# Kernel optimization log

Hardware: AMD Instinct MI355X
Metric: run time of the kernel (lower is better)

The kernel has to match this reference:

```python
import jax, jax.numpy as jnp
from jax import lax
import numpy as np

B, H, W = 8, 256, 256
NH = 128          # num_hiddens
NRH = 32          # num_residual_hiddens
K = 1024          # num_embeddings
D = 128           # embedding_dim
CC = 0.25         # commitment_cost


def setup_inputs() -> dict:
    key = jax.random.key(0)
    ks = jax.random.split(key, 18)

    def w(k, shape):
        fan_in = int(np.prod(shape[1:]))
        return (jax.random.normal(k, shape, jnp.float32) / np.sqrt(fan_in)).astype(jnp.float32)

    inp = {
        "x": jax.random.normal(ks[0], (B, 3, H, W), jnp.float32),
        # encoder
        "enc_c1": w(ks[1], (NH // 2, 3, 4, 4)),        # conv4x4 s2
        "enc_c2": w(ks[2], (NH, NH // 2, 4, 4)),       # conv4x4 s2
        "enc_c3": w(ks[3], (NH, NH, 3, 3)),            # conv3x3
        "enc_r1a": w(ks[4], (NRH, NH, 3, 3)),
        "enc_r1b": w(ks[5], (NH, NRH, 1, 1)),
        "enc_r2a": w(ks[6], (NRH, NH, 3, 3)),
        "enc_r2b": w(ks[7], (NH, NRH, 1, 1)),
        "pre_vq_w": w(ks[8], (D, NH, 1, 1)),
        # codebook: uniform(-1/K, 1/K) as in original init
        "codebook": jax.random.uniform(ks[9], (K, D), jnp.float32, -1.0 / K, 1.0 / K),
        # decoder
        "dec_c1": w(ks[10], (NH, D, 3, 3)),
        "dec_r1a": w(ks[11], (NRH, NH, 3, 3)),
        "dec_r1b": w(ks[12], (NH, NRH, 1, 1)),
        "dec_r2a": w(ks[13], (NRH, NH, 3, 3)),
        "dec_r2b": w(ks[14], (NH, NRH, 1, 1)),
        # ConvTranspose2d weight, torch layout [Cin, Cout, 4, 4]
        "dec_dc": w(ks[15], (NH, NH // 2, 4, 4)),
        "dec_c3": w(ks[16], (3, NH // 2, 3, 3)),
    }
    return inp


def _conv(x, w, s, p):
    return lax.conv_general_dilated(x, w, (s, s), ((p, p), (p, p)),
                                    dimension_numbers=("NCHW", "OIHW", "NCHW"))


def _deconv4x4_s2_p1(x, w_t):
    # torch ConvTranspose2d(k=4, s=2, p=1): flip kernel, swap in/out, lhs-dilate
    w = jnp.transpose(w_t[:, :, ::-1, ::-1], (1, 0, 2, 3))  # [Cout, Cin, 4, 4]
    return lax.conv_general_dilated(x, w, (1, 1), ((2, 2), (2, 2)),
                                    lhs_dilation=(2, 2),
                                    dimension_numbers=("NCHW", "OIHW", "NCHW"))


def _res_stack(x, r1a, r1b, r2a, r2b):
    for a, b in ((r1a, r1b), (r2a, r2b)):
        h = _conv(jax.nn.relu(x), a, 1, 1)
        h = _conv(jax.nn.relu(h), b, 1, 0)
        x = x + h
    return jax.nn.relu(x)


def _resize1d_align(x, axis, out_size):
    n = x.shape[axis]
    pos = jnp.arange(out_size, dtype=jnp.float32) * ((n - 1) / (out_size - 1))
    lo = jnp.floor(pos).astype(jnp.int32)
    hi = jnp.minimum(lo + 1, n - 1)
    wt = (pos - lo.astype(jnp.float32)).astype(x.dtype)
    shape = [1] * x.ndim
    shape[axis] = out_size
    wt = wt.reshape(shape)
    return jnp.take(x, lo, axis=axis) * (1 - wt) + jnp.take(x, hi, axis=axis) * wt


def _upsample2x_bilinear_align(x):  # align_corners=True, separable
    x = _resize1d_align(x, 2, 2 * x.shape[2])
    return _resize1d_align(x, 3, 2 * x.shape[3])


def reference(x, enc_c1, enc_c2, enc_c3, enc_r1a, enc_r1b, enc_r2a, enc_r2b,
              pre_vq_w, codebook, dec_c1, dec_r1a, dec_r1b, dec_r2a, dec_r2b,
              dec_dc, dec_c3):
    # ---- encoder ----
    h = jax.nn.relu(_conv(x, enc_c1, 2, 1))
    h = jax.nn.relu(_conv(h, enc_c2, 2, 1))
    h = _conv(h, enc_c3, 1, 1)            # note: no relu here (matches source)
    h = _res_stack(h, enc_r1a, enc_r1b, enc_r2a, enc_r2b)
    z = _conv(h, pre_vq_w, 1, 0)          # [B, D, H/4, W/4]

    # ---- VQ (eval mode: no EMA update, q_latent_loss = 0) ----
    zp = jnp.transpose(z, (0, 2, 3, 1))               # [B, h, w, D]
    flat = zp.reshape(-1, D)                          # [N, D]
    dist = (jnp.sum(flat * flat, axis=1, keepdims=True)
            + jnp.sum(codebook * codebook, axis=1)
            - 2.0 * flat @ codebook.T)                # [N, K]
    idx = jnp.argmin(dist, axis=1)                    # [N]
    q = codebook[idx].reshape(zp.shape)               # gather lookup
    e_latent_loss = jnp.mean((lax.stop_gradient(q) - zp) ** 2)
    loss = CC * e_latent_loss
    q_st = zp + lax.stop_gradient(q - zp)             # straight-through
    counts = jnp.zeros((K,), jnp.float32).at[idx].add(1.0)
    avg_probs = counts / flat.shape[0]
    perplexity = jnp.exp(-jnp.sum(avg_probs * jnp.log(avg_probs + 1e-10)))
    quantized = jnp.transpose(q_st, (0, 3, 1, 2))     # [B, D, h, w]

    # ---- decoder ----
    d = _conv(quantized, dec_c1, 1, 1)
    d = _res_stack(d, dec_r1a, dec_r1b, dec_r2a, dec_r2b)
    d = jax.nn.relu(_deconv4x4_s2_p1(d, dec_dc))
    d = _upsample2x_bilinear_align(d)
    d = _conv(d, dec_c3, 1, 1)
    recon = 2.0 * jax.nn.sigmoid(d) - 1.0             # [B, 3, H, W]
    return loss, recon, perplexity
```

## Files before the change

### kernel.cpp

```cpp
#include <hip/hip_runtime.h>
#include <hip/hip_bf16.h>
#include <math.h>

#define CC_COST 0.25

typedef __attribute__((ext_vector_type(8))) short short8v;
typedef __attribute__((ext_vector_type(4))) float f32x4;
typedef __attribute__((ext_vector_type(16))) float f32x16;

__device__ __forceinline__ unsigned short f2bf(float f) {
    unsigned u = __float_as_uint(f);
    unsigned r = (u + 0x7FFFu + ((u >> 16) & 1u)) >> 16;
    return (unsigned short)r;
}
__device__ __forceinline__ float bf2f(unsigned short h) {
    return __uint_as_float(((unsigned)h) << 16);
}


struct WtJobs {
    const float* src[15];
    float* dst[15];
    int cout[15], cin[15], kk[15], kind[15];
    int blk0[16];
};

__global__ void wt_batch_k(WtJobs J)
{
    int blk = blockIdx.x;
    int j = 0;
    while (j < 14 && blk >= J.blk0[j + 1]) ++j;
    int i = (blk - J.blk0[j]) * 256 + threadIdx.x;
    int total = J.cout[j] * J.cin[j] * J.kk[j];
    if (i >= total) return;
    const float* src = J.src[j];
    float* dst = J.dst[j];
    int kind = J.kind[j];
    if (kind == 0) {
        int Cout = J.cout[j], Cin = J.cin[j], KK = J.kk[j];
        int oc = i % Cout; int t2 = i / Cout; int t = t2 % KK; int c = t2 / KK;
        dst[i] = src[(oc * Cin + c) * KK + t];
    } else {
        int o = i % 3; int t = (i / 3) % 9; int c = i / 27;
        dst[i] = src[(o * 64 + c) * 9 + t];
    }
}

__global__ void wt_split_k(const float* __restrict__ w,
                           unsigned short* __restrict__ whi,
                           unsigned short* __restrict__ wlo)
{
    int i = blockIdx.x * 256 + threadIdx.x;
    if (i >= 147456) return;
    int ci = i & 15;
    int oc = (i >> 4) & 127;
    int rest = i >> 11;
    int cb = rest & 7;
    int tap = rest >> 3;
    float v = w[(oc * 128 + cb * 16 + ci) * 9 + tap];
    unsigned short h = f2bf(v);
    whi[i] = h;
    wlo[i] = f2bf(v - bf2f(h));
}

__global__ void wt_split4_k(const float* __restrict__ w,
                            unsigned short* __restrict__ whi,
                            unsigned short* __restrict__ wlo)
{
    int i = blockIdx.x * 256 + threadIdx.x;
    if (i >= 131072) return;
    int t = i & 15;
    int oc = (i >> 4) & 127;
    int rest = i >> 11;
    int cb = rest & 3;
    int tap = rest >> 2;
    float v = w[(oc * 64 + cb * 16 + t) * 16 + tap];
    unsigned short h = f2bf(v);
    whi[i] = h;
    wlo[i] = f2bf(v - bf2f(h));
}

__global__ void wt_split_dc_k(const float* __restrict__ w,
                              unsigned short* __restrict__ whi,
                              unsigned short* __restrict__ wlo)
{
    int i = blockIdx.x * 256 + threadIdx.x;
    if (i >= 131072) return;
    int ci = i & 15;
    int oc = (i >> 4) & 63;
    int cb = (i >> 10) & 7;
    int kx = (i >> 13) & 3;
    int ky = i >> 15;
    float v = w[((size_t)(cb * 16 + ci) * 64 + oc) * 16 + ky * 4 + kx];
    unsigned short h = f2bf(v);
    whi[i] = h;
    wlo[i] = f2bf(v - bf2f(h));
}

__global__ void wt_split_r_k(const float* __restrict__ w,
                             unsigned short* __restrict__ whi,
                             unsigned short* __restrict__ wlo)
{
    int i = blockIdx.x * 256 + threadIdx.x;
    if (i >= 36864) return;
    int k5 = i & 31;
    int oc = (i >> 5) & 31;
    int cb = (i >> 10) & 3;
    int tap = i >> 12;
    float v = w[(oc * 128 + cb * 32 + k5) * 9 + tap];
    unsigned short h = f2bf(v);
    whi[i] = h;
    wlo[i] = f2bf(v - bf2f(h));
}

__global__ void wt_split_1x1_k(const float* __restrict__ w,
                               unsigned short* __restrict__ whi,
                               unsigned short* __restrict__ wlo)
{
    int i = blockIdx.x * 256 + threadIdx.x;
    if (i >= 4096) return;
    int ci = i & 15;
    int oc = (i >> 4) & 127;
    int kk = i >> 11;
    float v = w[oc * 32 + kk * 16 + ci];
    unsigned short h = f2bf(v);
    whi[i] = h;
    wlo[i] = f2bf(v - bf2f(h));
}

__global__ __launch_bounds__(512) void conv3x3_mfma(
    const float* __restrict__ in,
    const unsigned short* __restrict__ whi,
    const unsigned short* __restrict__ wlo,
    float* __restrict__ out)
{
    constexpr int CST = 40;
    __shared__ unsigned short ls_hi[4 * 68 * CST];
    __shared__ unsigned short ls_lo[4 * 68 * CST];

    int tid = threadIdx.x;
    int lane = tid & 63;
    int w = tid >> 6;
    int myrow = w & 1;
    int oc0 = (w >> 1) * 32;
    int y0 = (blockIdx.x & 31) * 2;
    int b  = blockIdx.x >> 5;
    int ln31 = lane & 31;
    int lhf  = lane >> 5;

    f32x16 acc0 = {};
    f32x16 acc1 = {};

    const float* inb = in + (size_t)b * 128 * 4096;

    for (int chunk = 0; chunk < 4; ++chunk) {
        int c0 = chunk * 32;
        __syncthreads();
        for (int i = tid; i < 4 * 66 * 16; i += 512) {
            int x = i % 66;
            int t = i / 66;
            int cp = t & 15;
            int r = t >> 4;
            int gy = y0 - 1 + r, gx = x - 1;
            float v0 = 0.f, v1 = 0.f;
            if ((unsigned)gy < 64u && (unsigned)gx < 64u) {
                const float* p = inb + (size_t)(c0 + 2 * cp) * 4096 + gy * 64 + gx;
                v0 = p[0];
                v1 = p[4096];
            }
            unsigned short h0 = f2bf(v0), h1 = f2bf(v1);
            unsigned short l0 = f2bf(v0 - bf2f(h0)), l1 = f2bf(v1 - bf2f(h1));
            int a = (r * 68 + x) * CST + 2 * cp;
            *reinterpret_cast<unsigned int*>(&ls_hi[a]) = (unsigned)h0 | ((unsigned)h1 << 16);
            *reinterpret_cast<unsigned int*>(&ls_lo[a]) = (unsigned)l0 | ((unsigned)l1 << 16);
        }
        __syncthreads();

        #pragma unroll
        for (int tap = 0; tap < 9; ++tap) {
            int dy = tap / 3, dx = tap - 3 * (tap / 3);
            int rbase = (myrow + dy) * 68;
            #pragma unroll
            for (int cb = 0; cb < 2; ++cb) {
                int cbg = chunk * 2 + cb;
                size_t wofs = (((size_t)tap * 8 + cbg) * 128 + oc0 + ln31) * 16 + lhf * 8;
                short8v ah = *reinterpret_cast<const short8v*>(whi + wofs);
                short8v al = *reinterpret_cast<const short8v*>(wlo + wofs);
                int k0 = cb * 16 + lhf * 8;
                int xo0 = (rbase + ln31 + dx) * CST + k0;
                int xo1 = (rbase + 32 + ln31 + dx) * CST + k0;
                short8v bh0 = *reinterpret_cast<const short8v*>(&ls_hi[xo0]);
                short8v bl0 = *reinterpret_cast<const short8v*>(&ls_lo[xo0]);
                short8v bh1 = *reinterpret_cast<const short8v*>(&ls_hi[xo1]);
                short8v bl1 = *reinterpret_cast<const short8v*>(&ls_lo[xo1]);
                acc0 = __builtin_amdgcn_mfma_f32_32x32x16_bf16(ah, bh0, acc0, 0, 0, 0);
                acc1 = __builtin_amdgcn_mfma_f32_32x32x16_bf16(ah, bh1, acc1, 0, 0, 0);
                acc0 = __builtin_amdgcn_mfma_f32_32x32x16_bf16(ah, bl0, acc0, 0, 0, 0);
                acc1 = __builtin_amdgcn_mfma_f32_32x32x16_bf16(ah, bl1, acc1, 0, 0, 0);
                acc0 = __builtin_amdgcn_mfma_f32_32x32x16_bf16(al, bh0, acc0, 0, 0, 0);
                acc1 = __builtin_amdgcn_mfma_f32_32x32x16_bf16(al, bh1, acc1, 0, 0, 0);
            }
        }
    }

    float* ob = out + (size_t)b * 128 * 4096 + (size_t)(y0 + myrow) * 64;
    #pragma unroll
    for (int r = 0; r < 16; ++r) {
        int oc = oc0 + (r & 3) + 8 * (r >> 2) + 4 * lhf;
        ob[(size_t)oc * 4096 + ln31]      = acc0[r];
        ob[(size_t)oc * 4096 + 32 + ln31] = acc1[r];
    }
}

__global__ __launch_bounds__(512) void conv4x4s2_mfma(
    const float* __restrict__ in,
    const unsigned short* __restrict__ whi,
    const unsigned short* __restrict__ wlo,
    float* __restrict__ out)
{
    constexpr int CST = 24;
    __shared__ unsigned short lsEh[6 * 65 * CST];
    __shared__ unsigned short lsEl[6 * 65 * CST];
    __shared__ unsigned short lsOh[6 * 65 * CST];
    __shared__ unsigned short lsOl[6 * 65 * CST];

    int tid = threadIdx.x;
    int lane = tid & 63;
    int w = tid >> 6;
    int myrow = w & 1;
    int oc0 = (w >> 1) * 32;
    int y0 = (blockIdx.x & 31) * 2;
    int b  = blockIdx.x >> 5;
    int ln31 = lane & 31;
    int lhf  = lane >> 5;

    f32x16 acc0 = {};
    f32x16 acc1 = {};

    const float* inb = in + (size_t)b * 64 * 16384;

    for (int cb = 0; cb < 4; ++cb) {
        int c0 = cb * 16;
        __syncthreads();
        for (int i = tid; i < 12480; i += 512) {
            int gxi = i % 130; int t2 = i / 130;
            int r = t2 % 6; int cc = t2 / 6;
            int gx = gxi - 1;
            int gy = 2 * y0 - 1 + r;
            float v = 0.f;
            if ((unsigned)gy < 128u && (unsigned)gx < 128u)
                v = inb[(size_t)(c0 + cc) * 16384 + gy * 128 + gx];
            unsigned short h = f2bf(v);
            unsigned short l = f2bf(v - bf2f(h));
            if (gx & 1) {
                int a = (r * 65 + ((gx + 1) >> 1)) * CST + cc;
                lsOh[a] = h; lsOl[a] = l;
            } else {
                int a = (r * 65 + (gx >> 1)) * CST + cc;
                lsEh[a] = h; lsEl[a] = l;
            }
        }
        __syncthreads();

        #pragma unroll
        for (int tap = 0; tap < 16; ++tap) {
            int ky = tap >> 2, kx = tap & 3;
            int ridx = 2 * myrow + ky;
            int dlt = kx >> 1;
            const unsigned short* ph = (kx & 1) ? lsEh : lsOh;
            const unsigned short* pl = (kx & 1) ? lsEl : lsOl;
            size_t aoff = ((size_t)((tap * 4 + cb) * 128 + oc0 + ln31)) * 16 + lhf * 8;
            short8v ah = *reinterpret_cast<const short8v*>(whi + aoff);
            short8v al = *reinterpret_cast<const short8v*>(wlo + aoff);
            int base0 = (ridx * 65 + ln31 + dlt) * CST + lhf * 8;
            int base1 = (ridx * 65 + 32 + ln31 + dlt) * CST + lhf * 8;
            short8v bh0 = *reinterpret_cast<const short8v*>(ph + base0);
            short8v bl0 = *reinterpret_cast<const short8v*>(pl + base0);
            short8v bh1 = *reinterpret_cast<const short8v*>(ph + base1);
            short8v bl1 = *reinterpret_cast<const short8v*>(pl + base1);
            acc0 = __builtin_amdgcn_mfma_f32_32x32x16_bf16(ah, bh0, acc0, 0, 0, 0);
            acc1 = __builtin_amdgcn_mfma_f32_32x32x16_bf16(ah, bh1, acc1, 0, 0, 0);
            acc0 = __builtin_amdgcn_mfma_f32_32x32x16_bf16(ah, bl0, acc0, 0, 0, 0);
            acc1 = __builtin_amdgcn_mfma_f32_32x32x16_bf16(ah, bl1, acc1, 0, 0, 0);
            acc0 = __builtin_amdgcn_mfma_f32_32x32x16_bf16(al, bh0, acc0, 0, 0, 0);
            acc1 = __builtin_amdgcn_mfma_f32_32x32x16_bf16(al, bh1, acc1, 0, 0, 0);
        }
    }

    int y = y0 + myrow;
    float* ob = out + (size_t)b * 128 * 4096 + (size_t)y * 64;
    #pragma unroll
    for (int r = 0; r < 16; ++r) {
        int oc = oc0 + (r & 3) + 8 * (r >> 2) + 4 * lhf;
        ob[(size_t)oc * 4096 + ln31]      = fmaxf(acc0[r], 0.f);
        ob[(size_t)oc * 4096 + 32 + ln31] = fmaxf(acc1[r], 0.f);
    }
}

__global__ __launch_bounds__(512) void deconv_mfma(
    const float* __restrict__ in,
    const unsigned short* __restrict__ whi,
    const unsigned short* __restrict__ wlo,
    float* __restrict__ out)
{
    constexpr int CST = 40;
    __shared__ unsigned short ls_hi[3 * 68 * CST];
    __shared__ unsigned short ls_lo[3 * 68 * CST];

    int tid = threadIdx.x;
    int lane = tid & 63;
    int w = tid >> 6;
    int myrow = w & 1;
    int oc0 = ((w >> 1) & 1) * 32;
    int oxp = w >> 2;
    int yb = blockIdx.x & 63;
    int b  = blockIdx.x >> 6;
    int ln31 = lane & 31;
    int lhf  = lane >> 5;

    f32x16 acc0 = {};
    f32x16 acc1 = {};

    const float* inb = in + (size_t)b * 128 * 4096;

    for (int chunk = 0; chunk < 4; ++chunk) {
        int c0 = chunk * 32;
        __syncthreads();
        for (int i = tid; i < 3 * 66 * 16; i += 512) {
            int x = i % 66;
            int t = i / 66;
            int cp = t & 15;
            int r = t >> 4;
            int gy = yb - 1 + r, gx = x - 1;
            float v0 = 0.f, v1 = 0.f;
            if ((unsigned)gy < 64u && (unsigned)gx < 64u) {
                const float* p = inb + (size_t)(c0 + 2 * cp) * 4096 + gy * 64 + gx;
                v0 = fmaxf(p[0], 0.f);
                v1 = fmaxf(p[4096], 0.f);
            }
            unsigned short h0 = f2bf(v0), h1 = f2bf(v1);
            unsigned short l0 = f2bf(v0 - bf2f(h0)), l1 = f2bf(v1 - bf2f(h1));
            int a = (r * 68 + x) * CST + 2 * cp;
            *reinterpret_cast<unsigned int*>(&ls_hi[a]) = (unsigned)h0 | ((unsigned)h1 << 16);
            *reinterpret_cast<unsigned int*>(&ls_lo[a]) = (unsigned)l0 | ((unsigned)l1 << 16);
        }
        __syncthreads();

        #pragma unroll
        for (int tki = 0; tki < 2; ++tki) {
            int ky = (1 - myrow) + 2 * tki;
            int ldsrow = 1 + myrow - tki;
            #pragma unroll
            for (int txi = 0; txi < 2; ++txi) {
                int kx = (1 - oxp) + 2 * txi;
                int dlt = oxp - txi;
                #pragma unroll
                for (int cb = 0; cb < 2; ++cb) {
                    int cbg = chunk * 2 + cb;
                    size_t aoff = ((size_t)(((ky * 4 + kx) * 8 + cbg) * 64 + oc0 + ln31)) * 16 + lhf * 8;
                    short8v ah = *reinterpret_cast<const short8v*>(whi + aoff);
                    short8v al = *reinterpret_cast<const short8v*>(wlo + aoff);
                    int k0 = cb * 16 + lhf * 8;
                    int xo0 = (ldsrow * 68 + ln31 + dlt + 1) * CST + k0;
                    int xo1 = (ldsrow * 68 + 32 + ln31 + dlt + 1) * CST + k0;
                    short8v bh0 = *reinterpret_cast<const short8v*>(&ls_hi[xo0]);
                    short8v bl0 = *reinterpret_cast<const short8v*>(&ls_lo[xo0]);
                    short8v bh1 = *reinterpret_cast<const short8v*>(&ls_hi[xo1]);
                    short8v bl1 = *reinterpret_cast<const short8v*>(&ls_lo[xo1]);
                    acc0 = __builtin_amdgcn_mfma_f32_32x32x16_bf16(ah, bh0, acc0, 0, 0, 0);
                    acc1 = __builtin_amdgcn_mfma_f32_32x32x16_bf16(ah, bh1, acc1, 0, 0, 0);
                    acc0 = __builtin_amdgcn_mfma_f32_32x32x16_bf16(ah, bl0, acc0, 0, 0, 0);
                    acc1 = __builtin_amdgcn_mfma_f32_32x32x16_bf16(ah, bl1, acc1, 0, 0, 0);
                    acc0 = __builtin_amdgcn_mfma_f32_32x32x16_bf16(al, bh0, acc0, 0, 0, 0);
                    acc1 = __builtin_amdgcn_mfma_f32_32x32x16_bf16(al, bh1, acc1, 0, 0, 0);
                }
            }
        }
    }

    int oy = 2 * yb + myrow;
    float* ob = out + (size_t)b * 64 * 16384 + (size_t)oy * 128;
    #pragma unroll
    for (int r = 0; r < 16; ++r) {
        int oc = oc0 + (r & 3) + 8 * (r >> 2) + 4 * lhf;
        ob[(size_t)oc * 16384 + oxp + 2 * ln31]      = fmaxf(acc0[r], 0.f);
        ob[(size_t)oc * 16384 + oxp + 64 + 2 * ln31] = fmaxf(acc1[r], 0.f);
    }
}

__global__ __launch_bounds__(512) void fused_res_k(
    const float* __restrict__ in,
    const unsigned short* __restrict__ whi,
    const unsigned short* __restrict__ wlo,
    const unsigned short* __restrict__ w1hi,
    const unsigned short* __restrict__ w1lo,
    float* __restrict__ out)
{
    constexpr int CST = 40;
    __shared__ unsigned short ls_hi[3 * 68 * CST];
    __shared__ unsigned short ls_lo[3 * 68 * CST];

    int tid = threadIdx.x;
    int lane = tid & 63;
    int w = tid >> 6;
    int oc0 = (w & 1) * 16;
    int px0 = (w >> 1) * 16;
    int y = blockIdx.x & 63;
    int b = blockIdx.x >> 6;
    int n16 = lane & 15;
    int kk4 = lane >> 4;
    int ln31 = lane & 31;
    int lhf = lane >> 5;

    f32x4 acc = {};
    const float* inb = in + (size_t)b * 128 * 4096;

    for (int cb = 0; cb < 4; ++cb) {
        int c0 = cb * 32;
        __syncthreads();
        for (int i = tid; i < 3 * 66 * 16; i += 512) {
            int x = i % 66;
            int t = i / 66;
            int cp = t & 15;
            int r = t >> 4;
            int gy = y - 1 + r, gx = x - 1;
            float v0 = 0.f, v1 = 0.f;
            if ((unsigned)gy < 64u && (unsigned)gx < 64u) {
                const float* p = inb + (size_t)(c0 + 2 * cp) * 4096 + gy * 64 + gx;
                v0 = fmaxf(p[0], 0.f);
                v1 = fmaxf(p[4096], 0.f);
            }
            unsigned short h0 = f2bf(v0), h1 = f2bf(v1);
            unsigned short l0 = f2bf(v0 - bf2f(h0)), l1 = f2bf(v1 - bf2f(h1));
            int a = (r * 68 + x) * CST + 2 * cp;
            *reinterpret_cast<unsigned int*>(&ls_hi[a]) = (unsigned)h0 | ((unsigned)h1 << 16);
            *reinterpret_cast<unsigned int*>(&ls_lo[a]) = (unsigned)l0 | ((unsigned)l1 << 16);
        }
        __syncthreads();

        #pragma unroll
        for (int tap = 0; tap < 9; ++tap) {
            int dy = tap / 3, dx = tap - 3 * (tap / 3);
            size_t aoff = ((size_t)((tap * 4 + cb) * 32 + oc0 + n16)) * 32 + kk4 * 8;
            short8v ah = *reinterpret_cast<const short8v*>(whi + aoff);
            short8v al = *reinterpret_cast<const short8v*>(wlo + aoff);
            int xo = (dy * 68 + px0 + n16 + dx) * CST + kk4 * 8;
            short8v bh = *reinterpret_cast<const short8v*>(&ls_hi[xo]);
            short8v bl = *reinterpret_cast<const short8v*>(&ls_lo[xo]);
            acc = __builtin_amdgcn_mfma_f32_16x16x32_bf16(ah, bh, acc, 0, 0, 0);
            acc = __builtin_amdgcn_mfma_f32_16x16x32_bf16(ah, bl, acc, 0, 0, 0);
            acc = __builtin_amdgcn_mfma_f32_16x16x32_bf16(al, bh, acc, 0, 0, 0);
        }
    }

    __syncthreads();
    #pragma unroll
    for (int r = 0; r < 4; ++r) {
        int ch = oc0 + kk4 * 4 + r;
        int px = px0 + n16;
        float v = fmaxf(acc[r], 0.f);
        unsigned short h = f2bf(v);
        ls_hi[px * CST + ch] = h;
        ls_lo[px * CST + ch] = f2bf(v - bf2f(h));
    }
    __syncthreads();

    int oc1 = (w & 3) * 32;
    int pxt = (w >> 2) * 32;
    f32x16 acc2 = {};
    #pragma unroll
    for (int kk = 0; kk < 2; ++kk) {
        size_t aoff = ((size_t)(kk * 128 + oc1 + ln31)) * 16 + lhf * 8;
        short8v ah = *reinterpret_cast<const short8v*>(w1hi + aoff);
        short8v al = *reinterpret_cast<const short8v*>(w1lo + aoff);
        int boff = (pxt + ln31) * CST + kk * 16 + lhf * 8;
        short8v bh = *reinterpret_cast<const short8v*>(&ls_hi[boff]);
        short8v bl = *reinterpret_cast<const short8v*>(&ls_lo[boff]);
        acc2 = __builtin_amdgcn_mfma_f32_32x32x16_bf16(ah, bh, acc2, 0, 0, 0);
        acc2 = __builtin_amdgcn_mfma_f32_32x32x16_bf16(ah, bl, acc2, 0, 0, 0);
        acc2 = __builtin_amdgcn_mfma_f32_32x32x16_bf16(al, bh, acc2, 0, 0, 0);
    }

    float* ob = out + (size_t)b * 128 * 4096 + (size_t)y * 64;
    const float* rb = inb + (size_t)y * 64;
    #pragma unroll
    for (int r = 0; r < 16; ++r) {
        int oc = oc1 + (r & 3) + 8 * (r >> 2) + 4 * lhf;
        size_t o = (size_t)oc * 4096 + pxt + ln31;
        ob[o] = rb[o] + acc2[r];
    }
}

template<int CIN, int COUT, int CC, bool IN_RELU, bool ADD_RES>
__global__ __launch_bounds__(256) void conv1x1_k(
    const float* __restrict__ in, const float* __restrict__ wT,
    const float* __restrict__ res, float* __restrict__ out)
{
    static_assert(COUT == 128, "tile assumes 128");
    __shared__ __align__(16) float ls_in[CC][64];
    __shared__ __align__(16) float ls_w[CC][COUT];
    int tid = threadIdx.x;
    int pxg = tid & 7, ocg = tid >> 3;
    int x0 = pxg * 8, oc0 = ocg * 4;
    int y = blockIdx.x & 63, b = blockIdx.x >> 6;

    float acc[4][8];
    #pragma unroll
    for (int o = 0; o < 4; ++o)
        #pragma unroll
        for (int p = 0; p < 8; ++p) acc[o][p] = 0.f;

    for (int c0 = 0; c0 < CIN; c0 += CC) {
        __syncthreads();
        for (int i = tid; i < CC * 64; i += 256) {
            int xx = i & 63, cc = i >> 6;
            float v = in[(((size_t)b * CIN + c0 + cc) * 64 + y) * 64 + xx];
            if (IN_RELU) v = fmaxf(v, 0.f);
            ls_in[cc][xx] = v;
        }
        const float* wsrc = wT + (size_t)c0 * COUT;
        for (int i = tid; i < CC * COUT; i += 256)
            (&ls_w[0][0])[i] = wsrc[i];
        __syncthreads();

        for (int cc = 0; cc < CC; ++cc) {
            float rv[8];
            const float* base = &ls_in[cc][x0];
            float4 v0 = *reinterpret_cast<const float4*>(base);
            float4 v1 = *reinterpret_cast<const float4*>(base + 4);
            rv[0]=v0.x; rv[1]=v0.y; rv[2]=v0.z; rv[3]=v0.w;
            rv[4]=v1.x; rv[5]=v1.y; rv[6]=v1.z; rv[7]=v1.w;
            float4 w4 = *reinterpret_cast<const float4*>(&ls_w[cc][oc0]);
            float wv[4] = {w4.x, w4.y, w4.z, w4.w};
            #pragma unroll
            for (int p = 0; p < 8; ++p)
                #pragma unroll
                for (int o = 0; o < 4; ++o)
                    acc[o][p] = fmaf(rv[p], wv[o], acc[o][p]);
        }
    }
    #pragma unroll
    for (int o = 0; o < 4; ++o) {
        float* op = out + (((size_t)b * COUT + oc0 + o) * 64 + y) * 64 + x0;
        const float* rp = res + (((size_t)b * COUT + oc0 + o) * 64 + y) * 64 + x0;
        #pragma unroll
        for (int q = 0; q < 2; ++q) {
            float4 v = make_float4(acc[o][4*q], acc[o][4*q+1],
                                   acc[o][4*q+2], acc[o][4*q+3]);
            if (ADD_RES) {
                float4 r4 = *reinterpret_cast<const float4*>(rp + 4 * q);
                v.x += r4.x; v.y += r4.y; v.z += r4.z; v.w += r4.w;
            }
            *reinterpret_cast<float4*>(op + 4 * q) = v;
        }
    }
}

template<int CIN, int COUT, int WOUT, int CC, int OCB, int WOC, int NSLICE>
__global__ __launch_bounds__(256) void conv4x4s2_k(
    const float* __restrict__ in, const float* __restrict__ wT,
    float* __restrict__ out)
{
    constexpr int WIN = WOUT * 2;
    constexpr int NPXG = WOUT / 8, NOCG = COUT / OCB;
    static_assert(NPXG * NOCG == 256, "bad tile");
    constexpr int WUSE = 2 * WOUT + 2;
    constexpr int PADLEN = ((WUSE + (WUSE / 16 + 1) * 4) + 3) & ~3;
    __shared__ __align__(16) float ls_in[CC][4][PADLEN];
    __shared__ __align__(16) float ls_w[CC][16][COUT];

    int tid = threadIdx.x;
    int pxg = tid % NPXG, ocg = tid / NPXG;
    int x0 = pxg * 8, oc0 = ocg * OCB;
    int blk = blockIdx.x;
    int y = blk % WOUT; int rest = blk / WOUT;
    int slice = rest % NSLICE; int b = rest / NSLICE;
    int oc_base = slice * COUT;
    const float* inb = in + (size_t)b * CIN * WIN * WIN;

    float acc[OCB][8];
    #pragma unroll
    for (int o = 0; o < OCB; ++o)
        #pragma unroll
        for (int p = 0; p < 8; ++p) acc[o][p] = 0.f;

    for (int c0 = 0; c0 < CIN; c0 += CC) {
        __syncthreads();
        for (int i = tid; i < CC * 4 * WUSE; i += 256) {
            int xx = i % WUSE; int t = i / WUSE; int r = t & 3; int cc = t >> 2;
            int gy = 2 * y - 1 + r, gx = xx - 1;
            float v = 0.f;
            if ((unsigned)gy < (unsigned)WIN && (unsigned)gx < (unsigned)WIN)
                v = inb[(c0 + cc) * WIN * WIN + gy * WIN + gx];
            ls_in[cc][r][xx + ((xx >> 4) << 2)] = v;
        }
        const float* wsrc = wT + (size_t)c0 * 16 * WOC + oc_base;
        for (int i = tid; i < CC * 16 * COUT; i += 256) {
            int o = i % COUT; int tt = (i / COUT) % 16; int cc = i / (16 * COUT);
            ls_w[cc][tt][o] = wsrc[(cc * 16 + tt) * WOC + o];
        }
        __syncthreads();

        for (int cc = 0; cc < CC; ++cc) {
            const float* lw = &ls_w[cc][0][0];
            #pragma unroll
            for (int ky = 0; ky < 4; ++ky) {
                float rv[18];
                const float* base = &ls_in[cc][ky][20 * pxg];
                #pragma unroll
                for (int q = 0; q < 4; ++q) {
                    float4 v = *reinterpret_cast<const float4*>(base + 4 * q);
                    rv[4*q]=v.x; rv[4*q+1]=v.y; rv[4*q+2]=v.z; rv[4*q+3]=v.w;
                }
                rv[16] = base[20]; rv[17] = base[21];
                #pragma unroll
                for (int kx = 0; kx < 4; ++kx) {
                    const float* wp = lw + (ky * 4 + kx) * COUT + oc0;
                    float wv[OCB];
                    if constexpr (OCB == 4) {
                        float4 w4 = *reinterpret_cast<const float4*>(wp);
                        wv[0]=w4.x; wv[1]=w4.y; wv[2]=w4.z; wv[3]=w4.w;
                    } else {
                        float2 w2 = *reinterpret_cast<const float2*>(wp);
                        wv[0]=w2.x; wv[1]=w2.y;
                    }
                    #pragma unroll
                    for (int p = 0; p < 8; ++p) {
                        float iv = rv[2 * p + kx];
                        #pragma unroll
                        for (int o = 0; o < OCB; ++o)
                            acc[o][p] = fmaf(iv, wv[o], acc[o][p]);
                    }
                }
            }
        }
    }
    #pragma unroll
    for (int o = 0; o < OCB; ++o) {
        float* op = out + (((size_t)b * (COUT * NSLICE) + oc_base + oc0 + o) * WOUT + y) * WOUT + x0;
        #pragma unroll
        for (int q = 0; q < 2; ++q) {
            float4 v = make_float4(fmaxf(acc[o][4*q],0.f), fmaxf(acc[o][4*q+1],0.f),
                                   fmaxf(acc[o][4*q+2],0.f), fmaxf(acc[o][4*q+3],0.f));
            *reinterpret_cast<float4*>(op + 4 * q) = v;
        }
    }
}

template<int CC>
__global__ __launch_bounds__(256) void upconv_k(
    const float* __restrict__ in,
    const float* __restrict__ wT3,
    float* __restrict__ out)
{
    __shared__ __align__(16) float ls_u[CC][4][132];
    __shared__ float ls_w[64 * 27];
    __shared__ float xfx[132];
    __shared__ int   xloT[132];

    int tid = threadIdx.x;
    int row = tid >> 7;
    int pxl = tid & 127;
    int blk = blockIdx.x;
    int xh = blk & 1;
    int yblk = (blk >> 1) & 127;
    int b = blk >> 8;
    int xbase = xh * 128;
    int y0 = yblk * 2, y = y0 + row;
    const float SCL = 127.0f / 255.0f;
    const float* hb = in + (size_t)b * 64 * 16384;

    for (int i = tid; i < 1728; i += 256) ls_w[i] = wT3[i];
    if (tid < 130) {
        int ux = xbase - 1 + tid;
        bool v = ((unsigned)ux < 256u);
        float px = (v ? ux : 0) * SCL;
        int lo = (int)px;
        xloT[tid] = lo;
        xfx[tid] = v ? (px - (float)lo) : -1.0f;
    }

    float acc[3] = {0.f, 0.f, 0.f};

    for (int c0 = 0; c0 < 64; c0 += CC) {
        __syncthreads();
        for (int i = tid; i < CC * 4 * 130; i += 256) {
            int xx = i % 130; int t = i / 130; int r = t & 3; int cc = t >> 2;
            int uy = y0 - 1 + r;
            float v = 0.f;
            float fx = xfx[xx];
            if ((unsigned)uy < 256u && fx >= 0.f) {
                float py = uy * SCL;
                int ylo = (int)py; int yhi = min(ylo + 1, 127); float fy = py - (float)ylo;
                int lo = xloT[xx]; int hi = min(lo + 1, 127);
                const float* hp = hb + (size_t)(c0 + cc) * 16384 + ylo * 128;
                const float* hq = hb + (size_t)(c0 + cc) * 16384 + yhi * 128;
                float a = hp[lo], b2 = hp[hi], c2 = hq[lo], d2 = hq[hi];
                float top = a + (b2 - a) * fx;
                float bot = c2 + (d2 - c2) * fx;
                v = top + (bot - top) * fy;
            }
            ls_u[cc][r][xx] = v;
        }
        __syncthreads();

        for (int cc = 0; cc < CC; ++cc) {
            #pragma unroll
            for (int j = 0; j < 3; ++j) {
                const float* urow = &ls_u[cc][row + j][pxl];
                float r0 = urow[0], r1 = urow[1], r2 = urow[2];
                const float* wb = &ls_w[((c0 + cc) * 9 + j * 3) * 3];
                acc[0] = fmaf(r0, wb[0], acc[0]);
                acc[1] = fmaf(r0, wb[1], acc[1]);
                acc[2] = fmaf(r0, wb[2], acc[2]);
                acc[0] = fmaf(r1, wb[3], acc[0]);
                acc[1] = fmaf(r1, wb[4], acc[1]);
                acc[2] = fmaf(r1, wb[5], acc[2]);
                acc[0] = fmaf(r2, wb[6], acc[0]);
                acc[1] = fmaf(r2, wb[7], acc[1]);
                acc[2] = fmaf(r2, wb[8], acc[2]);
            }
        }
    }
    int x0 = xbase + pxl;
    #pragma unroll
    for (int o = 0; o < 3; ++o) {
        float v = 2.f / (1.f + expf(-acc[o])) - 1.f;
        out[(((size_t)b * 3 + o) * 256 + y) * 256 + x0] = v;
    }
}

__global__ void prep_codebook(const float* __restrict__ cb,
                              unsigned short* __restrict__ cbh,
                              unsigned short* __restrict__ cbl,
                              float* __restrict__ ce2,
                              unsigned int* __restrict__ counts)
{
    int k = blockIdx.x * 256 + threadIdx.x;
    if (k >= 1024) return;
    float s = 0.f;
    for (int d = 0; d < 128; ++d) {
        float v = cb[k * 128 + d];
        s = fmaf(v, v, s);
        unsigned short h = f2bf(v);
        int kk = d >> 4, t = d & 15;
        cbh[(kk * 1024 + k) * 16 + t] = h;
        cbl[(kk * 1024 + k) * 16 + t] = f2bf(v - bf2f(h));
    }
    ce2[k] = s;
    counts[k] = 0u;
}

__global__ __launch_bounds__(512) void vq_fused(
    const float* __restrict__ z, const float* __restrict__ cb,
    const unsigned short* __restrict__ cbh,
    const unsigned short* __restrict__ cbl,
    const float* __restrict__ ce2,
    unsigned int* __restrict__ counts, float* __restrict__ q,
    double* __restrict__ partial)
{
    constexpr int ZP = 136;
    __shared__ unsigned short zh[64 * ZP];
    __shared__ unsigned short zlo[64 * ZP];
    __shared__ float ce2l[1024];
    __shared__ float cmbd[4][2][32];
    __shared__ int   cmbi[4][2][32];
    __shared__ int sidx[64];
    __shared__ float red[8];

    int tid = threadIdx.x;
    int lane = tid & 63;
    int w = tid >> 6;
    int pxg = w & 1;
    int cgrp = w >> 1;
    int ln31 = lane & 31;
    int lhf = lane >> 5;
    int p0g = blockIdx.x * 64;
    int b = p0g >> 12;
    int p0 = p0g & 4095;

    for (int i = tid; i < 8192; i += 512) {
        int d = i >> 6, px = i & 63;
        float v = z[((size_t)b * 128 + d) * 4096 + p0 + px];
        unsigned short h = f2bf(v);
        zh[px * ZP + d]  = h;
        zlo[px * ZP + d] = f2bf(v - bf2f(h));
    }
    for (int i = tid; i < 1024; i += 512) ce2l[i] = ce2[i];
    __syncthreads();

    int pxrow = pxg * 32 + ln31;
    short8v zfh[8], zfl[8];
    #pragma unroll
    for (int kk = 0; kk < 8; ++kk) {
        int off = pxrow * ZP + kk * 16 + lhf * 8;
        zfh[kk] = *reinterpret_cast<const short8v*>(&zh[off]);
        zfl[kk] = *reinterpret_cast<const short8v*>(&zlo[off]);
    }

    float best = 3.4e38f; int bidx = 0;
    #pragma unroll
    for (int ct = 0; ct < 8; ++ct) {
        int c0 = cgrp * 256 + ct * 32;
        f32x16 acc = {};
        #pragma unroll
        for (int kk = 0; kk < 8; ++kk) {
            size_t aoff = ((size_t)(kk * 1024 + c0 + ln31)) * 16 + lhf * 8;
            short8v ah = *reinterpret_cast<const short8v*>(cbh + aoff);
            short8v al = *reinterpret_cast<const short8v*>(cbl + aoff);
            acc = __builtin_amdgcn_mfma_f32_32x32x16_bf16(ah, zfh[kk], acc, 0, 0, 0);
            acc = __builtin_amdgcn_mfma_f32_32x32x16_bf16(ah, zfl[kk], acc, 0, 0, 0);
            acc = __builtin_amdgcn_mfma_f32_32x32x16_bf16(al, zfh[kk], acc, 0, 0, 0);
        }
        #pragma unroll
        for (int r = 0; r < 16; ++r) {
            int code = c0 + (r & 3) + 8 * (r >> 2) + 4 * lhf;
            float dist = ce2l[code] - 2.f * acc[r];
            if (dist < best || (dist == best && code < bidx)) { best = dist; bidx = code; }
        }
    }
    {
        float ob = __shfl_xor(best, 32);
        int   oi = __shfl_xor(bidx, 32);
        if (ob < best || (ob == best && oi < bidx)) { best = ob; bidx = oi; }
    }
    if (lane < 32) { cmbd[cgrp][pxg][lane] = best; cmbi[cgrp][pxg][lane] = bidx; }
    __syncthreads();
    if (tid < 64) {
        int pg = tid >> 5, l = tid & 31;
        float bv = cmbd[0][pg][l]; int bi = cmbi[0][pg][l];
        #pragma unroll
        for (int g = 1; g < 4; ++g) {
            float ov = cmbd[g][pg][l]; int oi = cmbi[g][pg][l];
            if (ov < bv || (ov == bv && oi < bi)) { bv = ov; bi = oi; }
        }
        sidx[pg * 32 + l] = bi;
        atomicAdd(&counts[bi], 1u);
    }
    __syncthreads();

    int pix = tid & 63, dg = tid >> 6;
    int kidx = sidx[pix];
    const float* crow = cb + (size_t)kidx * 128 + dg * 16;
    float sq = 0.f;
    size_t zbase = ((size_t)b * 128 + dg * 16) * 4096 + p0 + pix;
    #pragma unroll
    for (int ii = 0; ii < 4; ++ii) {
        float4 c4 = *reinterpret_cast<const float4*>(crow + 4 * ii);
        float vals[4] = {c4.x, c4.y, c4.z, c4.w};
        #pragma unroll
        for (int jj = 0; jj < 4; ++jj) {
            int dl = ii * 4 + jj;
            float qv = vals[jj];
            float zv = z[zbase + (size_t)dl * 4096];
            float df = qv - zv;
            sq = fmaf(df, df, sq);
            q[zbase + (size_t)dl * 4096] = qv;
        }
    }
    #pragma unroll
    for (int off = 32; off > 0; off >>= 1) sq += __shfl_xor(sq, off);
    if (lane == 0) red[w] = sq;
    __syncthreads();
    if (tid == 0) {
        double s = 0.0;
        #pragma unroll
        for (int ww = 0; ww < 8; ++ww) s += (double)red[ww];
        partial[blockIdx.x] = s;
    }
}

__global__ __launch_bounds__(256) void finalize_kernel(
    const double* __restrict__ partial, const unsigned int* __restrict__ counts,
    float* __restrict__ dout)
{
    __shared__ double sd[256];
    __shared__ double lossSh;
    int tid = threadIdx.x;
    double s = 0.0;
    for (int i = tid; i < 512; i += 256) s += partial[i];
    sd[tid] = s; __syncthreads();
    for (int off = 128; off > 0; off >>= 1) {
        if (tid < off) sd[tid] += sd[tid + off];
        __syncthreads();
    }
    if (tid == 0) lossSh = CC_COST * sd[0] / 4194304.0;
    __syncthreads();

    double h = 0.0;
    for (int k = tid; k < 1024; k += 256) {
        double pp = (double)counts[k] / 32768.0;
        h += pp * log(pp + 1e-10);
    }
    sd[tid] = h; __syncthreads();
    for (int off = 128; off > 0; off >>= 1) {
        if (tid < off) sd[tid] += sd[tid + off];
        __syncthreads();
    }
    if (tid == 0) {
        dout[0]       = (float)lossSh;
        dout[1572865] = (float)exp(-sd[0]);
    }
}

extern "C" void kernel_launch(void* const* d_in, const int* in_sizes, int n_in,
                              void* d_out, int out_size, void* d_ws, size_t ws_size,
                              hipStream_t stream)
{
    const float* x        = (const float*)d_in[0];
    const float* enc_c1   = (const float*)d_in[1];
    const float* enc_c2   = (const float*)d_in[2];
    const float* enc_c3   = (const float*)d_in[3];
    const float* enc_r1a  = (const float*)d_in[4];
    const float* enc_r1b  = (const float*)d_in[5];
    const float* enc_r2a  = (const float*)d_in[6];
    const float* enc_r2b  = (const float*)d_in[7];
    const float* pre_vq_w = (const float*)d_in[8];
    const float* codebook = (const float*)d_in[9];
    const float* dec_c1   = (const float*)d_in[10];
    const float* dec_r1a  = (const float*)d_in[11];
    const float* dec_r1b  = (const float*)d_in[12];
    const float* dec_r2a  = (const float*)d_in[13];
    const float* dec_r2b  = (const float*)d_in[14];
    const float* dec_dc   = (const float*)d_in[15];
    const float* dec_c3   = (const float*)d_in[16];
    float* dout = (float*)d_out;

    char* wsp = (char*)d_ws;
    auto alloc = [&](size_t bytes) {
        void* p = (void*)wsp;
        wsp += (bytes + 255) & ~(size_t)255;
        return p;
    };
    float* h1   = (float*)alloc(8ull*64*128*128*4);
    float* bufA = (float*)alloc(8ull*128*64*64*4);
    float* bufB = (float*)alloc(8ull*128*64*64*4);
    unsigned short* cbh = (unsigned short*)alloc(131072*2);
    unsigned short* cbl = (unsigned short*)alloc(131072*2);
    float* ce2  = (float*)alloc(1024*4);
    unsigned int* counts = (unsigned int*)alloc(1024*4);
    double* partial = (double*)alloc(512*8);
    float* wt_ec1  = (float*)alloc(3072*4);
    float* wt_pvq  = (float*)alloc(16384*4);
    float* wt_dc3  = (float*)alloc(1728*4);
    unsigned short* w3hi_e = (unsigned short*)alloc(147456*2);
    unsigned short* w3lo_e = (unsigned short*)alloc(147456*2);
    unsigned short* w3hi_d = (unsigned short*)alloc(147456*2);
    unsigned short* w3lo_d = (unsigned short*)alloc(147456*2);
    unsigned short* w4hi   = (unsigned short*)alloc(131072*2);
    unsigned short* w4lo   = (unsigned short*)alloc(131072*2);
    unsigned short* wdchi  = (unsigned short*)alloc(131072*2);
    unsigned short* wdclo  = (unsigned short*)alloc(131072*2);
    unsigned short* wr1aeh = (unsigned short*)alloc(36864*2);
    unsigned short* wr1ael = (unsigned short*)alloc(36864*2);
    unsigned short* wr2aeh = (unsigned short*)alloc(36864*2);
    unsigned short* wr2ael = (unsigned short*)alloc(36864*2);
    unsigned short* wr1adh = (unsigned short*)alloc(36864*2);
    unsigned short* wr1adl = (unsigned short*)alloc(36864*2);
    unsigned short* wr2adh = (unsigned short*)alloc(36864*2);
    unsigned short* wr2adl = (unsigned short*)alloc(36864*2);
    unsigned short* w1e1h  = (unsigned short*)alloc(4096*2);
    unsigned short* w1e1l  = (unsigned short*)alloc(4096*2);
    unsigned short* w1e2h  = (unsigned short*)alloc(4096*2);
    unsigned short* w1e2l  = (unsigned short*)alloc(4096*2);
    unsigned short* w1d1h  = (unsigned short*)alloc(4096*2);
    unsigned short* w1d1l  = (unsigned short*)alloc(4096*2);
    unsigned short* w1d2h  = (unsigned short*)alloc(4096*2);
    unsigned short* w1d2l  = (unsigned short*)alloc(4096*2);
    float* zb = bufA;
    float* qb = h1;

    prep_codebook<<<4, 256, 0, stream>>>(codebook, cbh, cbl, ce2, counts);

    WtJobs J;
    const float* srcs[3] = {enc_c1, pre_vq_w, dec_c3};
    float* dsts[3] = {wt_ec1, wt_pvq, wt_dc3};
    int couts[3] = {64, 128, 3};
    int cins[3]  = {3, 128, 64};
    int kks[3]   = {16, 1, 9};
    int kinds[3] = {0, 0, 2};
    int off = 0;
    for (int j = 0; j < 3; ++j) {
        J.src[j] = srcs[j]; J.dst[j] = dsts[j];
        J.cout[j] = couts[j]; J.cin[j] = cins[j]; J.kk[j] = kks[j];
        J.kind[j] = kinds[j];
        J.blk0[j] = off;
        off += (couts[j] * cins[j] * kks[j] + 255) / 256;
    }
    J.blk0[3] = off;
    for (int j = 4; j < 16; ++j) J.blk0[j] = off + 1000000;
    wt_batch_k<<<off, 256, 0, stream>>>(J);
    wt_split_k<<<576, 256, 0, stream>>>(enc_c3, w3hi_e, w3lo_e);
    wt_split_k<<<576, 256, 0, stream>>>(dec_c1, w3hi_d, w3lo_d);
    wt_split4_k<<<512, 256, 0, stream>>>(enc_c2, w4hi, w4lo);
    wt_split_dc_k<<<512, 256, 0, stream>>>(dec_dc, wdchi, wdclo);
    wt_split_r_k<<<144, 256, 0, stream>>>(enc_r1a, wr1aeh, wr1ael);
    wt_split_r_k<<<144, 256, 0, stream>>>(enc_r2a, wr2aeh, wr2ael);
    wt_split_r_k<<<144, 256, 0, stream>>>(dec_r1a, wr1adh, wr1adl);
    wt_split_r_k<<<144, 256, 0, stream>>>(dec_r2a, wr2adh, wr2adl);
    wt_split_1x1_k<<<16, 256, 0, stream>>>(enc_r1b, w1e1h, w1e1l);
    wt_split_1x1_k<<<16, 256, 0, stream>>>(enc_r2b, w1e2h, w1e2l);
    wt_split_1x1_k<<<16, 256, 0, stream>>>(dec_r1b, w1d1h, w1d1l);
    wt_split_1x1_k<<<16, 256, 0, stream>>>(dec_r2b, w1d2h, w1d2l);

    conv4x4s2_k<3, 64, 128, 3, 4, 64, 1><<<1024, 256, 0, stream>>>(x, wt_ec1, h1);
    conv4x4s2_mfma<<<256, 512, 0, stream>>>(h1, w4hi, w4lo, bufA);
    conv3x3_mfma<<<256, 512, 0, stream>>>(bufA, w3hi_e, w3lo_e, bufB);
    fused_res_k<<<512, 512, 0, stream>>>(bufB, wr1aeh, wr1ael, w1e1h, w1e1l, bufA);
    fused_res_k<<<512, 512, 0, stream>>>(bufA, wr2aeh, wr2ael, w1e2h, w1e2l, bufB);
    conv1x1_k<128, 128, 32, true, false><<<512, 256, 0, stream>>>(bufB, wt_pvq, bufB, zb);

    vq_fused<<<512, 512, 0, stream>>>(zb, codebook, cbh, cbl, ce2, counts, qb, partial);

    conv3x3_mfma<<<256, 512, 0, stream>>>(qb, w3hi_d, w3lo_d, bufA);
    fused_res_k<<<512, 512, 0, stream>>>(bufA, wr1adh, wr1adl, w1d1h, w1d1l, bufB);
    fused_res_k<<<512, 512, 0, stream>>>(bufB, wr2adh, wr2adl, w1d2h, w1d2l, bufA);
    deconv_mfma<<<512, 512, 0, stream>>>(bufA, wdchi, wdclo, h1);
    upconv_k<4><<<2048, 256, 0, stream>>>(h1, wt_dc3, dout + 1);

    finalize_kernel<<<1, 256, 0, stream>>>(partial, counts, dout);
}
```

Before: 759.5 us.

## Move final upsample+3x3 conv onto bf16x3 MFMA with padded output channels

```diff
diff --git a/kernel.cpp b/kernel.cpp
--- a/kernel.cpp
+++ b/kernel.cpp
@@ -123,6 +123,26 @@
     int oc = (i >> 4) & 127;
     int kk = i >> 11;
     float v = w[oc * 32 + kk * 16 + ci];
+    unsigned short h = f2bf(v);
+    whi[i] = h;
+    wlo[i] = f2bf(v - bf2f(h));
+}
+
+__global__ void wt_split_up_k(const float* __restrict__ w,
+                              unsigned short* __restrict__ whi,
+                              unsigned short* __restrict__ wlo)
+{
+    int i = blockIdx.x * 256 + threadIdx.x;
+    if (i >= 18432) return;
+    int ci = i & 15;
+    int oc = (i >> 4) & 31;
+    int cb = (i >> 9) & 3;
+    int tap = i >> 11;
+    float v = 0.f;
+    if (oc < 3) {
+        int ch = cb * 16 + ci;
+        v = w[(oc * 64 + ch) * 9 + tap];
+    }
     unsigned short h = f2bf(v);
     whi[i] = h;
     wlo[i] = f2bf(v - bf2f(h));
@@ -647,31 +667,35 @@
     }
 }
 
-template<int CC>
-__global__ __launch_bounds__(256) void upconv_k(
+__global__ __launch_bounds__(512) void upconv_mfma(
     const float* __restrict__ in,
-    const float* __restrict__ wT3,
+    const unsigned short* __restrict__ whi,
+    const unsigned short* __restrict__ wlo,
     float* __restrict__ out)
 {
-    __shared__ __align__(16) float ls_u[CC][4][132];
-    __shared__ float ls_w[64 * 27];
-    __shared__ float xfx[132];
-    __shared__ int   xloT[132];
+    constexpr int CST = 24;
+    __shared__ unsigned short ls_hi[6 * 68 * CST];
+    __shared__ unsigned short ls_lo[6 * 68 * CST];
+    __shared__ float xfx[68];
+    __shared__ int   xloT[68];
 
     int tid = threadIdx.x;
-    int row = tid >> 7;
-    int pxl = tid & 127;
+    int lane = tid & 63;
+    int w = tid >> 6;
+    int myrow = w & 3;
+    int pt = w >> 2;
     int blk = blockIdx.x;
-    int xh = blk & 1;
-    int yblk = (blk >> 1) & 127;
+    int xq = blk & 3;
+    int yblk = (blk >> 2) & 63;
     int b = blk >> 8;
-    int xbase = xh * 128;
-    int y0 = yblk * 2, y = y0 + row;
+    int xbase = xq * 64;
+    int y0 = yblk * 4;
+    int ln31 = lane & 31;
+    int lhf = lane >> 5;
     const float SCL = 127.0f / 255.0f;
     const float* hb = in + (size_t)b * 64 * 16384;
 
-    for (int i = tid; i < 1728; i += 256) ls_w[i] = wT3[i];
-    if (tid < 130) {
+    if (tid < 68) {
         int ux = xbase - 1 + tid;
         bool v = ((unsigned)ux < 256u);
         float px = (v ? ux : 0) * SCL;
@@ -680,53 +704,66 @@
         xfx[tid] = v ? (px - (float)lo) : -1.0f;
     }
 
-    float acc[3] = {0.f, 0.f, 0.f};
-
-    for (int c0 = 0; c0 < 64; c0 += CC) {
-        __syncthreads();
-        for (int i = tid; i < CC * 4 * 130; i += 256) {
-            int xx = i % 130; int t = i / 130; int r = t & 3; int cc = t >> 2;
+    f32x16 acc = {};
+
+    for (int chunk = 0; chunk < 4; ++chunk) {
+        int c0 = chunk * 16;
+        __syncthreads();
+        for (int i = tid; i < 6 * 68 * 8; i += 512) {
+            int xx = i % 68; int t = i / 68; int cp = t & 7; int r = t >> 3;
             int uy = y0 - 1 + r;
-            float v = 0.f;
+            float v0 = 0.f, v1 = 0.f;
             float fx = xfx[xx];
             if ((unsigned)uy < 256u && fx >= 0.f) {
                 float py = uy * SCL;
-                int ylo = (int)py; int yhi = min(ylo + 1, 127); float fy = py - (float)ylo;
+                int ylo = (int)py; int yhi = min(ylo + 1, 127);
+                float fy = py - (float)ylo;
                 int lo = xloT[xx]; int hi = min(lo + 1, 127);
-                const float* hp = hb + (size_t)(c0 + cc) * 16384 + ylo * 128;
-                const float* hq = hb + (size_t)(c0 + cc) * 16384 + yhi * 128;
-                float a = hp[lo], b2 = hp[hi], c2 = hq[lo], d2 = hq[hi];
+                const float* hp = hb + (size_t)(c0 + 2 * cp) * 16384;
+                const float* p0 = hp + ylo * 128;
+                const float* p1 = hp + yhi * 128;
+                float a = p0[lo], b2 = p0[hi], c2 = p1[lo], d2 = p1[hi];
                 float top = a + (b2 - a) * fx;
                 float bot = c2 + (d2 - c2) * fx;
-                v = top + (bot - top) * fy;
+                v0 = top + (bot - top) * fy;
+                const float* q0 = p0 + 16384;
+                const float* q1 = p1 + 16384;
+                float a2 = q0[lo], b3 = q0[hi], c3 = q1[lo], d3 = q1[hi];
+                float top2 = a2 + (b3 - a2) * fx;
+                float bot2 = c3 + (d3 - c3) * fx;
+                v1 = top2 + (bot2 - top2) * fy;
             }
-            ls_u[cc][r][xx] = v;
-        }
-        __syncthreads();
-
-        for (int cc = 0; cc < CC; ++cc) {
-            #pragma unroll
-            for (int j = 0; j < 3; ++j) {
-                const float* urow = &ls_u[cc][row + j][pxl];
-                float r0 = urow[0], r1 = urow[1], r2 = urow[2];
-                const float* wb = &ls_w[((c0 + cc) * 9 + j * 3) * 3];
-                acc[0] = fmaf(r0, wb[0], acc[0]);
-                acc[1] = fmaf(r0, wb[1], acc[1]);
-                acc[2] = fmaf(r0, wb[2], acc[2]);
-                acc[0] = fmaf(r1, wb[3], acc[0]);
-                acc[1] = fmaf(r1, wb[4], acc[1]);
-                acc[2] = fmaf(r1, wb[5], acc[2]);
-                acc[0] = fmaf(r2, wb[6], acc[0]);
-                acc[1] = fmaf(r2, wb[7], acc[1]);
-                acc[2] = fmaf(r2, wb[8], acc[2]);
-            }
-        }
-    }
-    int x0 = xbase + pxl;
-    #pragma unroll
-    for (int o = 0; o < 3; ++o) {
-        float v = 2.f / (1.f + expf(-acc[o])) - 1.f;
-        out[(((size_t)b * 3 + o) * 256 + y) * 256 + x0] = v;
+            unsigned short h0 = f2bf(v0), h1 = f2bf(v1);
+            unsigned short l0 = f2bf(v0 - bf2f(h0)), l1 = f2bf(v1 - bf2f(h1));
+            int a = (r * 68 + xx) * CST + 2 * cp;
+            *reinterpret_cast<unsigned int*>(&ls_hi[a]) = (unsigned)h0 | ((unsigned)h1 << 16);
+            *reinterpret_cast<unsigned int*>(&ls_lo[a]) = (unsigned)l0 | ((unsigned)l1 << 16);
+        }
+        __syncthreads();
+
+        #pragma unroll
+        for (int tap = 0; tap < 9; ++tap) {
+            int dy = tap / 3, dx = tap - 3 * (tap / 3);
+            size_t aoff = ((size_t)((tap * 4 + chunk) * 32 + ln31)) * 16 + lhf * 8;
+            short8v ah = *reinterpret_cast<const short8v*>(whi + aoff);
+            short8v al = *reinterpret_cast<const short8v*>(wlo + aoff);
+            int boff = ((myrow + dy) * 68 + pt * 32 + ln31 + dx) * CST + lhf * 8;
+            short8v bh = *reinterpret_cast<const short8v*>(&ls_hi[boff]);
+            short8v bl = *reinterpret_cast<const short8v*>(&ls_lo[boff]);
+            acc = __builtin_amdgcn_mfma_f32_32x32x16_bf16(ah, bh, acc, 0, 0, 0);
+            acc = __builtin_amdgcn_mfma_f32_32x32x16_bf16(ah, bl, acc, 0, 0, 0);
+            acc = __builtin_amdgcn_mfma_f32_32x32x16_bf16(al, bh, acc, 0, 0, 0);
+        }
+    }
+
+    if (lhf == 0) {
+        int y = y0 + myrow;
+        int x0 = xbase + pt * 32 + ln31;
+        #pragma unroll
+        for (int r = 0; r < 3; ++r) {
+            float v = 2.f / (1.f + expf(-acc[r])) - 1.f;
+            out[(((size_t)b * 3 + r) * 256 + y) * 256 + x0] = v;
+        }
     }
 }
 
@@ -942,7 +979,6 @@
     double* partial = (double*)alloc(512*8);
     float* wt_ec1  = (float*)alloc(3072*4);
     float* wt_pvq  = (float*)alloc(16384*4);
-    float* wt_dc3  = (float*)alloc(1728*4);
     unsigned short* w3hi_e = (unsigned short*)alloc(147456*2);
     unsigned short* w3lo_e = (unsigned short*)alloc(147456*2);
     unsigned short* w3hi_d = (unsigned short*)alloc(147456*2);
@@ -967,28 +1003,30 @@
     unsigned short* w1d1l  = (unsigned short*)alloc(4096*2);
     unsigned short* w1d2h  = (unsigned short*)alloc(4096*2);
     unsigned short* w1d2l  = (unsigned short*)alloc(4096*2);
+    unsigned short* wuph   = (unsigned short*)alloc(18432*2);
+    unsigned short* wupl   = (unsigned short*)alloc(18432*2);
     float* zb = bufA;
     float* qb = h1;
 
     prep_codebook<<<4, 256, 0, stream>>>(codebook, cbh, cbl, ce2, counts);
 
     WtJobs J;
-    const float* srcs[3] = {enc_c1, pre_vq_w, dec_c3};
-    float* dsts[3] = {wt_ec1, wt_pvq, wt_dc3};
-    int couts[3] = {64, 128, 3};
-    int cins[3]  = {3, 128, 64};
-    int kks[3]   = {16, 1, 9};
-    int kinds[3] = {0, 0, 2};
+    const float* srcs[2] = {enc_c1, pre_vq_w};
+    float* dsts[2] = {wt_ec1, wt_pvq};
+    int couts[2] = {64, 128};
+    int cins[2]  = {3, 128};
+    int kks[2]   = {16, 1};
+    int kinds[2] = {0, 0};
     int off = 0;
-    for (int j = 0; j < 3; ++j) {
+    for (int j = 0; j < 2; ++j) {
         J.src[j] = srcs[j]; J.dst[j] = dsts[j];
         J.cout[j] = couts[j]; J.cin[j] = cins[j]; J.kk[j] = kks[j];
         J.kind[j] = kinds[j];
         J.blk0[j] = off;
         off += (couts[j] * cins[j] * kks[j] + 255) / 256;
     }
-    J.blk0[3] = off;
-    for (int j = 4; j < 16; ++j) J.blk0[j] = off + 1000000;
+    J.blk0[2] = off;
+    for (int j = 3; j < 16; ++j) J.blk0[j] = off + 1000000;
     wt_batch_k<<<off, 256, 0, stream>>>(J);
     wt_split_k<<<576, 256, 0, stream>>>(enc_c3, w3hi_e, w3lo_e);
     wt_split_k<<<576, 256, 0, stream>>>(dec_c1, w3hi_d, w3lo_d);
@@ -1002,6 +1040,7 @@
     wt_split_1x1_k<<<16, 256, 0, stream>>>(enc_r2b, w1e2h, w1e2l);
     wt_split_1x1_k<<<16, 256, 0, stream>>>(dec_r1b, w1d1h, w1d1l);
     wt_split_1x1_k<<<16, 256, 0, stream>>>(dec_r2b, w1d2h, w1d2l);
+    wt_split_up_k<<<72, 256, 0, stream>>>(dec_c3, wuph, wupl);
 
     conv4x4s2_k<3, 64, 128, 3, 4, 64, 1><<<1024, 256, 0, stream>>>(x, wt_ec1, h1);
     conv4x4s2_mfma<<<256, 512, 0, stream>>>(h1, w4hi, w4lo, bufA);
@@ -1016,7 +1055,7 @@
     fused_res_k<<<512, 512, 0, stream>>>(bufA, wr1adh, wr1adl, w1d1h, w1d1l, bufB);
     fused_res_k<<<512, 512, 0, stream>>>(bufB, wr2adh, wr2adl, w1d2h, w1d2l, bufA);
     deconv_mfma<<<512, 512, 0, stream>>>(bufA, wdchi, wdclo, h1);
-    upconv_k<4><<<2048, 256, 0, stream>>>(h1, wt_dc3, dout + 1);
+    upconv_mfma<<<2048, 512, 0, stream>>>(h1, wuph, wupl, dout + 1);
 
     finalize_kernel<<<1, 256, 0, stream>>>(partial, counts, dout);
 }
```

New measurement: 730.6 us. -3.8%, faster.
